# Optimization experiments

Hardware: AMD Instinct MI355X
Metric: run time of the kernel (lower is better)

## Reference

```python
import jax, jax.numpy as jnp
import numpy as np

P = 45007
VEC = 4            # default_vec in the triton kernel
BK = 32            # BLOCK_SIZE_K
BN = 32            # BLOCK_SIZE_N
REDN = 2           # reduction factor
IN_FEATURES = 4096
OUT_FEATURES = 4096
RED_IN = ((IN_FEATURES // REDN + BK - 1) // BK) * BK  # 2048


def build_full_idx(random_numbers, K, N, red_in, bk, bn, redn, vec):
    """Vectorized port of SSL.get_idx: flat indices into weight.flatten() for the
    expanded (K, N) weight (i.e. full_weight^T)."""
    R0 = random_numbers[0].astype(jnp.int32)
    R1 = random_numbers[1].astype(jnp.int32)
    R2 = random_numbers[2].astype(jnp.int32)
    R3 = random_numbers[3].astype(jnp.int32)
    ni = K // bk   # number of K blocks
    nj = N // bn   # number of N blocks
    i = jnp.arange(ni, dtype=jnp.int32)
    j = jnp.arange(nj, dtype=jnp.int32)
    it = i // redn                 # [ni]
    itin = i % redn                # [ni]
    h = R3 + R2 * j[None, :] + R1 * (it[:, None] + 1)   # [ni, nj]
    h1 = R0 * (itin + 1)                                 # [ni]
    offset = bk - ((h + h1[:, None]) * vec) % bk         # [ni, nj]
    locs = (offset[:, :, None] + jnp.arange(bk, dtype=jnp.int32)) % bk  # [ni, nj, bk]
    # row index into the compressed weight's reduced-K axis
    row_red = it[:, None, None] * bk + locs              # [ni, nj, bk]
    # reorder so k = i*bk + kk is the leading axis: (ni, bk, nj) -> (K, nj)
    row_red = jnp.transpose(row_red, (0, 2, 1)).reshape(K, nj)
    row_full = jnp.repeat(row_red, bn, axis=1)           # [K, N]
    n_idx = jnp.arange(N, dtype=jnp.int32)[None, :]
    return n_idx * red_in + row_full                     # flat index into weight.flatten()


def setup_inputs() -> dict:
    key = jax.random.key(0)
    k1, k2, k3 = jax.random.split(key, 3)
    x = jax.random.normal(k1, (4, 2048, IN_FEATURES), dtype=jnp.float32)
    # xavier_uniform over (out_features, red_in_features)
    bound_w = float(np.sqrt(6.0 / (OUT_FEATURES + RED_IN)))
    weight = jax.random.uniform(k2, (OUT_FEATURES, RED_IN), dtype=jnp.float32,
                                minval=-bound_w, maxval=bound_w)
    bound_b = 1.0 / float(np.sqrt(IN_FEATURES))
    bias = jax.random.uniform(k3, (OUT_FEATURES,), dtype=jnp.float32,
                              minval=-bound_b, maxval=bound_b)
    # random_numbers = cat([P], 3 ints in [0, P)); fixed representative values
    random_numbers = jnp.array([P, 12345, 6789, 23456], dtype=jnp.int32)
    return {"x": x, "weight": weight, "bias": bias, "random_numbers": random_numbers}


def reference(x, weight, bias, random_numbers):
    K = x.shape[-1]
    N = weight.shape[0]
    full_idx = build_full_idx(random_numbers, K, N, RED_IN, BK, BN, REDN, VEC)  # [K, N]
    w_full = weight.reshape(-1)[full_idx]            # [K, N] = expanded weight^T
    x2 = x.reshape(-1, K)                            # [M, K]
    y = x2 @ w_full + bias[None, :]                  # [M, N]
    return y.reshape(*x.shape[:-1], N)
```

## Files before the change

### kernel.cpp

```cpp
#include <hip/hip_runtime.h>

typedef __bf16 bf16x8 __attribute__((ext_vector_type(8)));
typedef float  f32x4  __attribute__((ext_vector_type(4)));
typedef unsigned short ushort8 __attribute__((ext_vector_type(8)));

#define KDIM  4096
#define NDIM  4096
#define REDIN 2048

static __device__ __forceinline__ unsigned short f2bf(float f) {
    return __builtin_bit_cast(unsigned short, (__bf16)f);
}

typedef __attribute__((address_space(3))) void       lds_void;
typedef const __attribute__((address_space(1))) void gbl_cvoid;

static __device__ __forceinline__ void gload16(const void* g, void* l) {
    __builtin_amdgcn_global_load_lds((gbl_cvoid*)g, (lds_void*)l, 16, 0, 0);
}

__global__ void prep_fused(const float* __restrict__ x, const float* __restrict__ w,
                           const int* __restrict__ rn,
                           unsigned short* __restrict__ xb, unsigned short* __restrict__ wx,
                           long n8x) {
    if (blockIdx.x < 2048) {
        long idx = (long)blockIdx.x * blockDim.x + threadIdx.x;
        long stride = (long)2048 * blockDim.x;
        for (long i = idx; i < n8x; i += stride) {
            const float4 a = ((const float4*)x)[2 * i];
            const float4 b = ((const float4*)x)[2 * i + 1];
            ushort8 s;
            s[0] = f2bf(a.x); s[1] = f2bf(a.y); s[2] = f2bf(a.z); s[3] = f2bf(a.w);
            s[4] = f2bf(b.x); s[5] = f2bf(b.y); s[6] = f2bf(b.z); s[7] = f2bf(b.w);
            ((ushort8*)xb)[i] = s;
        }
    } else {
        const int R0 = rn[0], R1 = rn[1], R2 = rn[2], R3 = rn[3];
        const long total = (long)NDIM * (KDIM / 8);
        long idx = (long)(blockIdx.x - 2048) * blockDim.x + threadIdx.x;
        long stride = (long)1024 * blockDim.x;
        for (long t = idx; t < total; t += stride) {
            const int kp = (int)(t & (KDIM / 8 - 1));
            const int n  = (int)(t >> 9);
            const int k0 = kp * 8;
            const int i  = k0 >> 5;
            const int kk0 = k0 & 31;
            const int it = i >> 1;
            const int h  = R3 + R2 * (n >> 5) + R1 * (it + 1) + R0 * ((i & 1) + 1);
            const int off = 32 - ((h << 2) & 31);
            const float* src = w + (long)n * REDIN + it * 32;
            ushort8 s;
#pragma unroll
            for (int q = 0; q < 8; ++q)
                s[q] = f2bf(src[(kk0 + q + off) & 31]);
            ((ushort8*)wx)[t] = s;
        }
    }
}


#define STAGE_H(MAT, T, HALF)                                               \
  {                                                                         \
    char* _d = (char*)lds##MAT + ((((T) & 1) * 2 + (HALF)) * 16384) + tid * 16; \
    const unsigned short* _s = src##MAT + (size_t)((HALF) * 128) * KDIM + (size_t)(T) * 64; \
    gload16(_s, _d);                                                        \
    gload16(_s + (size_t)64 * KDIM, _d + 8192);                             \
  }

#define READ_A(PA, MH)                                                      \
  _Pragma("unroll")                                                         \
  for (int _kk = 0; _kk < 2; ++_kk)                                         \
    _Pragma("unroll")                                                       \
    for (int _mf = 0; _mf < 4; ++_mf)                                       \
      a_[_kk][_mf] = *(const bf16x8*)((PA) + (MH) * 8192 + _mf * 2048 + (roff ^ (_kk << 6)));

#define READ_B(PB, NH)                                                      \
  _Pragma("unroll")                                                         \
  for (int _kk = 0; _kk < 2; ++_kk)                                         \
    _Pragma("unroll")                                                       \
    for (int _nf = 0; _nf < 2; ++_nf)                                       \
      b_##NH[_kk][_nf] = *(const bf16x8*)((PB) + (NH) * 4096 + _nf * 2048 + (roff ^ (_kk << 6)));

#define MFMA_Q(MH, NH)                                                      \
  __builtin_amdgcn_s_setprio(1);                                            \
  _Pragma("unroll")                                                         \
  for (int _kk = 0; _kk < 2; ++_kk)                                         \
    _Pragma("unroll")                                                       \
    for (int _mf = 0; _mf < 4; ++_mf)                                       \
      _Pragma("unroll")                                                     \
      for (int _nf = 0; _nf < 2; ++_nf)                                     \
        acc[(MH) * 4 + _mf][(NH) * 2 + _nf] = __builtin_amdgcn_mfma_f32_16x16x32_bf16( \
            a_[_kk][_mf], b_##NH[_kk][_nf], acc[(MH) * 4 + _mf][(NH) * 2 + _nf], 0, 0, 0); \
  __builtin_amdgcn_s_setprio(0);

#define SB __builtin_amdgcn_sched_barrier(0)
#define BAR __builtin_amdgcn_s_barrier()

#define GROUP(U, BUF, STG, VMSTR)                                           \
  {                                                                         \
    const char* paA = ldsAc + ((BUF) * 2 + wr) * 16384;                     \
    const char* pbB = ldsBc + ((BUF) * 2 + bh) * 16384 + bhw;               \
                                                                    \
    READ_A(paA, 0)                                                          \
    READ_B(pbB, 0)                                                          \
    if ((STG) >= 1) { STAGE_H(A, (U) + 1, 0); STAGE_H(A, (U) + 1, 1); }     \
    asm volatile("s_waitcnt lgkmcnt(4)" ::: "memory");                      \
    SB; BAR;                                                                \
    asm volatile("s_waitcnt lgkmcnt(0)" ::: "memory");                      \
    SB;                                                                     \
    MFMA_Q(0, 0)                                                            \
    SB;                                                                     \
                                                                    \
    READ_B(pbB, 1)                                                          \
    SB; BAR;                                                                \
    asm volatile("s_waitcnt lgkmcnt(0)" ::: "memory");                      \
    SB;                                                                     \
    MFMA_Q(0, 1)                                                            \
    SB;                                                                     \
                                                                    \
    READ_A(paA, 1)                                                          \
    if ((STG) >= 2) STAGE_H(B, (U) + 2, 0);                                 \
    SB; BAR;                                                                \
    asm volatile("s_waitcnt lgkmcnt(0)" ::: "memory");                      \
    SB;                                                                     \
    MFMA_Q(1, 1)                                                            \
    SB;                                                                     \
                                                                    \
    if ((STG) >= 2) STAGE_H(B, (U) + 2, 1);                                 \
    SB;                                                                     \
    MFMA_Q(1, 0)                                                            \
    asm volatile("s_waitcnt vmcnt(" VMSTR ")" ::: "memory");                \
    SB; BAR; SB;                                                            \
  }

__global__ __launch_bounds__(512, 2)
void gemm_bt256(const unsigned short* __restrict__ A,
                const unsigned short* __restrict__ B,
                const float* __restrict__ bias,
                float* __restrict__ out, int M)
{
    __shared__ __align__(16) unsigned short ldsA[2 * 2 * 8192];
    __shared__ __align__(16) unsigned short ldsB[2 * 2 * 8192];
    const char* ldsAc = (const char*)ldsA;
    const char* ldsBc = (const char*)ldsB;

    const int nwg = gridDim.x;
    const int bid = blockIdx.x;
    int swzb = bid;
    if ((nwg & 7) == 0) {
        const int cpx = nwg >> 3;
        swzb = (bid & 7) * cpx + (bid >> 3);
    }
    const int ntn = NDIM / 256;
    const int n0 = (swzb % ntn) * 256;
    const int m0 = (swzb / ntn) * 256;

    const int tid  = threadIdx.x;
    const int lane = tid & 63;
    const int wid  = tid >> 6;
    const int wr   = wid >> 2;
    const int wc   = wid & 3;
    const int bh   = wc >> 1;
    const int bhw  = (wc & 1) * 8192;
    const int lrow = lane & 15;
    const int g    = lane >> 4;

    const int roff = lrow * 128 + (((g ^ (lrow & 7)) & 7) << 4);

    const int srow = tid >> 3;
    const int sslot = (tid & 7) ^ (srow & 7);
    const unsigned short* srcA = A + (size_t)(m0 + srow) * KDIM + 8 * sslot;
    const unsigned short* srcB = B + (size_t)(n0 + srow) * KDIM + 8 * sslot;

    f32x4 acc[8][4];
#pragma unroll
    for (int m = 0; m < 8; ++m)
#pragma unroll
        for (int n = 0; n < 4; ++n)
            acc[m][n] = (f32x4)(0.0f);

    bf16x8 a_[2][4], b_0[2][2], b_1[2][2];

    STAGE_H(A, 0, 0);
    STAGE_H(A, 0, 1);
    STAGE_H(B, 0, 0);
    STAGE_H(B, 0, 1);
    STAGE_H(B, 1, 0);
    STAGE_H(B, 1, 1);
    asm volatile("s_waitcnt vmcnt(4)" ::: "memory");
    SB; BAR; SB;

    for (int u = 0; u < 62; u += 2) {
        GROUP(u,     0, 2, "4");
        GROUP(u + 1, 1, 2, "4");
    }
    GROUP(62, 0, 1, "0");
    GROUP(63, 1, 0, "0");

#pragma unroll
    for (int n = 0; n < 4; ++n) {
        const int col = n0 + wc * 64 + n * 16 + lrow;
        const float bv = bias[col];
#pragma unroll
        for (int m = 0; m < 8; ++m) {
            const size_t rbase = (size_t)(m0 + wr * 128 + m * 16 + (lane >> 4) * 4);
#pragma unroll
            for (int e = 0; e < 4; ++e)
                out[(rbase + e) * NDIM + col] = acc[m][n][e] + bv;
        }
    }
}

__global__ __launch_bounds__(256, 2)
void ssl_gemm_fused(const float* __restrict__ x, const float* __restrict__ w,
                    const float* __restrict__ bias, const int* __restrict__ rn,
                    float* __restrict__ out)
{
    __shared__ __align__(16) unsigned short As[128][40];
    __shared__ __align__(16) unsigned short Bs[128][40];

    const int R0 = rn[0], R1 = rn[1], R2 = rn[2], R3 = rn[3];
    const int tid = threadIdx.x;
    const int n0 = blockIdx.x * 128;
    const int m0 = blockIdx.y * 128;
    const int srow = tid >> 3;
    const int scol = (tid & 7) * 4;
    const int lane = tid & 63;
    const int wid  = tid >> 6;
    const int wr   = wid >> 1;
    const int wc   = wid & 1;
    const int lrow = lane & 15;
    const int lk   = (lane >> 4) * 8;

    f32x4 acc[4][4];
#pragma unroll
    for (int m = 0; m < 4; ++m)
#pragma unroll
        for (int n = 0; n < 4; ++n)
            acc[m][n] = (f32x4)(0.0f);

    for (int i = 0; i < KDIM / 32; ++i) {
        const int it   = i >> 1;
        const int k0   = i * 32;
#pragma unroll
        for (int p = 0; p < 4; ++p) {
            const int row = p * 32 + srow;
            const float4 v = *(const float4*)(x + (size_t)(m0 + row) * KDIM + k0 + scol);
            ushort4 s;
            s.x = f2bf(v.x); s.y = f2bf(v.y); s.z = f2bf(v.z); s.w = f2bf(v.w);
            *(ushort4*)&As[row][scol] = s;
        }
        const int hbase = R3 + R1 * (it + 1) + R0 * ((i & 1) + 1);
#pragma unroll
        for (int p = 0; p < 4; ++p) {
            const int nl = p * 32 + srow;
            const int j  = (n0 + nl) >> 5;
            const int off = 32 - (((hbase + R2 * j) << 2) & 31);
            const float4 v = *(const float4*)(w + (size_t)(n0 + nl) * REDIN + it * 32 + scol);
            Bs[nl][(scol + 0 - off) & 31] = f2bf(v.x);
            Bs[nl][(scol + 1 - off) & 31] = f2bf(v.y);
            Bs[nl][(scol + 2 - off) & 31] = f2bf(v.z);
            Bs[nl][(scol + 3 - off) & 31] = f2bf(v.w);
        }
        __syncthreads();

        bf16x8 af[4], bfr[4];
#pragma unroll
        for (int m = 0; m < 4; ++m)
            af[m] = *(const bf16x8*)&As[wr * 64 + m * 16 + lrow][lk];
#pragma unroll
        for (int n = 0; n < 4; ++n)
            bfr[n] = *(const bf16x8*)&Bs[wc * 64 + n * 16 + lrow][lk];
#pragma unroll
        for (int m = 0; m < 4; ++m)
#pragma unroll
            for (int n = 0; n < 4; ++n)
                acc[m][n] = __builtin_amdgcn_mfma_f32_16x16x32_bf16(af[m], bfr[n], acc[m][n], 0, 0, 0);
        __syncthreads();
    }

#pragma unroll
    for (int n = 0; n < 4; ++n) {
        const int col = n0 + wc * 64 + n * 16 + lrow;
        const float bv = bias[col];
#pragma unroll
        for (int m = 0; m < 4; ++m) {
            const int rbase = m0 + wr * 64 + m * 16 + (lane >> 4) * 4;
#pragma unroll
            for (int e = 0; e < 4; ++e)
                out[(size_t)(rbase + e) * NDIM + col] = acc[m][n][e] + bv;
        }
    }
}

extern "C" void kernel_launch(void* const* d_in, const int* in_sizes, int n_in,
                              void* d_out, int out_size, void* d_ws, size_t ws_size,
                              hipStream_t stream) {
    const float* x    = (const float*)d_in[0];
    const float* wgt  = (const float*)d_in[1];
    const float* bias = (const float*)d_in[2];
    const int*   rn   = (const int*)d_in[3];
    float* out = (float*)d_out;

    const int M = in_sizes[0] / KDIM;
    const size_t need = ((size_t)M * KDIM + (size_t)NDIM * KDIM) * sizeof(unsigned short);

    if (ws_size >= need && (M % 256) == 0) {
        unsigned short* xb = (unsigned short*)d_ws;
        unsigned short* wx = xb + (size_t)M * KDIM;

        prep_fused<<<3072, 256, 0, stream>>>(x, wgt, rn, xb, wx, (long)M * KDIM / 8);

        const int nwg = (NDIM / 256) * (M / 256);
        gemm_bt256<<<nwg, 512, 0, stream>>>(xb, wx, bias, out, M);
    } else {
        dim3 grid(NDIM / 128, M / 128);
        ssl_gemm_fused<<<grid, dim3(256), 0, stream>>>(x, wgt, bias, rn, out);
    }
}
```

Measured before the change: 272.8 us.

## Restructure LDS staging of A and B tiles for finer-grained prefetch overlap

Reorganizes the LDS layout and global-to-LDS staging in the bf16 GEMM. A tiles are now split into two 64-row phases and prefetched further ahead (half of tile u+2 is issued during tile u). B tiles are staged with a per-wave row mapping so each wave loads contiguous LDS chunks. The vmcnt waits are retuned to match the deeper in-flight load count. The aim is to spread global loads more evenly across the MFMA phases and hide more memory latency, at the cost of more outstanding loads and tighter synchronization correctness requirements.

```diff
diff --git a/kernel.cpp b/kernel.cpp
--- a/kernel.cpp
+++ b/kernel.cpp
@@ -59,12 +59,20 @@
 }
 
 
-#define STAGE_H(MAT, T, HALF)                                               \
+#define STAGE_A(T, PHI)                                                     \
   {                                                                         \
-    char* _d = (char*)lds##MAT + ((((T) & 1) * 2 + (HALF)) * 16384) + tid * 16; \
-    const unsigned short* _s = src##MAT + (size_t)((HALF) * 128) * KDIM + (size_t)(T) * 64; \
+    char* _d = (char*)ldsA + (((T) & 1) * 32768) + ((PHI) * 8192) + tid * 16; \
+    const unsigned short* _s = srcA + (size_t)((PHI) * 64) * KDIM + (size_t)(T) * 64; \
     gload16(_s, _d);                                                        \
-    gload16(_s + (size_t)64 * KDIM, _d + 8192);                             \
+    gload16(_s + (size_t)128 * KDIM, _d + 16384);                           \
+  }
+
+#define STAGE_B(T, PHI)                                                     \
+  {                                                                         \
+    char* _b = (char*)ldsB + (((T) & 1) * 32768) + ((PHI) * 4096);          \
+    const size_t _ko = (size_t)((PHI) * 32) * KDIM + (size_t)(T) * 64;      \
+    gload16(srcB0 + _ko, _b + boff0);                                       \
+    gload16(srcB1 + _ko, _b + boff1);                                       \
   }
 
 #define READ_A(PA, MH)                                                      \
@@ -96,14 +104,14 @@
 #define SB __builtin_amdgcn_sched_barrier(0)
 #define BAR __builtin_amdgcn_s_barrier()
 
-#define GROUP(U, BUF, STG, VMSTR)                                           \
+#define GROUP(U, BUF, STG, VM2, VM1)                                        \
   {                                                                         \
-    const char* paA = ldsAc + ((BUF) * 2 + wr) * 16384;                     \
-    const char* pbB = ldsBc + ((BUF) * 2 + bh) * 16384 + bhw;               \
+    const char* paA = ldsAc + (BUF) * 32768 + wr * 16384;                   \
+    const char* pbB = ldsBc + (BUF) * 32768 + bh * 16384 + bhw;             \
                                                                     \
     READ_A(paA, 0)                                                          \
     READ_B(pbB, 0)                                                          \
-    if ((STG) >= 1) { STAGE_H(A, (U) + 1, 0); STAGE_H(A, (U) + 1, 1); }     \
+    if ((STG) >= 1) STAGE_A((U) + 1, 1);                                    \
     asm volatile("s_waitcnt lgkmcnt(4)" ::: "memory");                      \
     SB; BAR;                                                                \
     asm volatile("s_waitcnt lgkmcnt(0)" ::: "memory");                      \
@@ -112,6 +120,8 @@
     SB;                                                                     \
                                                                     \
     READ_B(pbB, 1)                                                          \
+    if ((STG) >= 2) STAGE_A((U) + 2, 0);                                    \
+    asm volatile("s_waitcnt vmcnt(" VM2 ")" ::: "memory");                  \
     SB; BAR;                                                                \
     asm volatile("s_waitcnt lgkmcnt(0)" ::: "memory");                      \
     SB;                                                                     \
@@ -119,17 +129,17 @@
     SB;                                                                     \
                                                                     \
     READ_A(paA, 1)                                                          \
-    if ((STG) >= 2) STAGE_H(B, (U) + 2, 0);                                 \
+    if ((STG) >= 2) STAGE_B((U) + 2, 0);                                    \
     SB; BAR;                                                                \
     asm volatile("s_waitcnt lgkmcnt(0)" ::: "memory");                      \
     SB;                                                                     \
     MFMA_Q(1, 1)                                                            \
     SB;                                                                     \
                                                                     \
-    if ((STG) >= 2) STAGE_H(B, (U) + 2, 1);                                 \
+    if ((STG) >= 2) STAGE_B((U) + 2, 1);                                    \
     SB;                                                                     \
     MFMA_Q(1, 0)                                                            \
-    asm volatile("s_waitcnt vmcnt(" VMSTR ")" ::: "memory");                \
+    asm volatile("s_waitcnt vmcnt(" VM1 ")" ::: "memory");                  \
     SB; BAR; SB;                                                            \
   }
 
@@ -139,8 +149,8 @@
                 const float* __restrict__ bias,
                 float* __restrict__ out, int M)
 {
-    __shared__ __align__(16) unsigned short ldsA[2 * 2 * 8192];
-    __shared__ __align__(16) unsigned short ldsB[2 * 2 * 8192];
+    __shared__ __align__(16) unsigned short ldsA[2 * 16384];
+    __shared__ __align__(16) unsigned short ldsB[2 * 16384];
     const char* ldsAc = (const char*)ldsA;
     const char* ldsBc = (const char*)ldsB;
 
@@ -170,7 +180,15 @@
     const int srow = tid >> 3;
     const int sslot = (tid & 7) ^ (srow & 7);
     const unsigned short* srcA = A + (size_t)(m0 + srow) * KDIM + 8 * sslot;
-    const unsigned short* srcB = B + (size_t)(n0 + srow) * KDIM + 8 * sslot;
+
+    const int s0i = wid, s1i = wid + 8;
+    const int boff0 = (s0i >> 2) * 8192 + (s0i & 3) * 1024 + lane * 16;
+    const int boff1 = (s1i >> 2) * 8192 + (s1i & 3) * 1024 + lane * 16;
+    const int rB0 = (s0i >> 2) * 64 + (s0i & 3) * 8 + (lane >> 3);
+    const int rB1 = (s1i >> 2) * 64 + (s1i & 3) * 8 + (lane >> 3);
+    const int kslotB = (lane & 7) ^ (lane >> 3);
+    const unsigned short* srcB0 = B + (size_t)(n0 + rB0) * KDIM + 8 * kslotB;
+    const unsigned short* srcB1 = B + (size_t)(n0 + rB1) * KDIM + 8 * kslotB;
 
     f32x4 acc[8][4];
 #pragma unroll
@@ -181,21 +199,22 @@
 
     bf16x8 a_[2][4], b_0[2][2], b_1[2][2];
 
-    STAGE_H(A, 0, 0);
-    STAGE_H(A, 0, 1);
-    STAGE_H(B, 0, 0);
-    STAGE_H(B, 0, 1);
-    STAGE_H(B, 1, 0);
-    STAGE_H(B, 1, 1);
-    asm volatile("s_waitcnt vmcnt(4)" ::: "memory");
+    STAGE_A(0, 0);
+    STAGE_B(0, 0);
+    STAGE_B(0, 1);
+    STAGE_A(0, 1);
+    STAGE_A(1, 0);
+    STAGE_B(1, 0);
+    STAGE_B(1, 1);
+    asm volatile("s_waitcnt vmcnt(6)" ::: "memory");
     SB; BAR; SB;
 
     for (int u = 0; u < 62; u += 2) {
-        GROUP(u,     0, 2, "4");
-        GROUP(u + 1, 1, 2, "4");
-    }
-    GROUP(62, 0, 1, "0");
-    GROUP(63, 1, 0, "0");
+        GROUP(u,     0, 2, "10", "8");
+        GROUP(u + 1, 1, 2, "10", "8");
+    }
+    GROUP(62, 0, 1, "8", "2");
+    GROUP(63, 1, 0, "0", "0");
 
 #pragma unroll
     for (int n = 0; n < 4; ++n) {
```

Result: slower. 289.6 us (+6.2%).
